# Kernel optimization log

Hardware: AMD Instinct MI355X
Metric: run time of the kernel (lower is better)

The kernel has to match this reference:

```python
import jax, jax.numpy as jnp
import numpy as np

B, H, S, D = 2, 16, 2048, 64  # batch, heads, seq, head_dim (d_model=1024)


def setup_inputs() -> dict:
    key = jax.random.key(0)
    kq, kk, kv, kp, kl = jax.random.split(key, 5)
    q = jax.random.normal(kq, (B, H, S, D), dtype=jnp.float32)
    k = jax.random.normal(kk, (B, H, D, S), dtype=jnp.float32)  # pre-transposed keys
    v = jax.random.normal(kv, (B, H, S, D), dtype=jnp.float32)
    prev = jax.random.normal(kp, (B, H, S, S), dtype=jnp.float32)  # Realformer residual scores
    # tail padding: each batch element has a random valid length in [S//2, S]
    lengths = jax.random.randint(kl, (B,), S // 2, S + 1)
    key_padding_mask = jnp.arange(S)[None, :] >= lengths[:, None]  # [B,S] bool, True = pad
    # causal attention mask, True = disallowed
    attn_mask = jnp.triu(jnp.ones((S, S), dtype=bool), k=1)[None, None]  # [1,1,S,S]
    scale = jnp.asarray(D ** -0.5, dtype=jnp.float32)        # learnable (lsa=True)
    extra_scale = jnp.asarray(1.0, dtype=jnp.float32)        # learnable (lsa=True)
    return {"q": q, "k": k, "v": v, "prev": prev,
            "key_padding_mask": key_padding_mask, "attn_mask": attn_mask,
            "scale": scale, "extra_scale": extra_scale}


def reference(q, k, v, prev, key_padding_mask, attn_mask, scale, extra_scale):
    eff_scale = scale * jnp.clip(extra_scale, 0.01, 50.0)
    # q @ k (k already [B,H,D,S]) -> scores [B,H,S,S]
    attn_scores = jnp.einsum('bhqd,bhdk->bhqk', q, k) * eff_scale + prev
    attn_scores = jnp.where(attn_mask, -jnp.inf, attn_scores)
    attn_scores = jnp.where(key_padding_mask[:, None, None, :], -jnp.inf, attn_scores)
    attn_weights = jax.nn.softmax(attn_scores, axis=-1)  # dropout p=0.0 -> identity
    output = jnp.einsum('bhqk,bhkd->bhqd', attn_weights, v)
    # res_attention=True -> return scores too
    return output, attn_weights, attn_scores
```

## Files before the change

### kernel.cpp

```cpp
#include <hip/hip_runtime.h>
#include <math.h>

#define S_LEN 2048
#define D_DIM 64
#define OUT_O_OFF 0
#define OUT_W_OFF 4194304
#define OUT_S_OFF 138412032

#define MASK_VAL (-1.0e30f)

typedef const __attribute__((address_space(4))) float* cfp;

__device__ __forceinline__ void decode_tile(int bid, int& bh, int& qt, int& cc) {
    const int xr = bid & 7, r = bid >> 3;
    bh = xr * 4 + (r >> 9);
    const int rem = r & 511;
    qt = rem >> 3;
    cc = rem & 7;
}

__device__ __forceinline__ void decode_row(int bid, int& bh, int& qt) {
    const int xr = bid & 7, r = bid >> 3;
    bh = xr * 4 + (r >> 6);
    qt = 63 - (r & 63);
}

__device__ __forceinline__ void fill_tile(float* dst_bh, int q0, int c0,
                                          float val, int t) {
    const float4 v4 = make_float4(val, val, val, val);
#pragma unroll
    for (int jj = 0; jj < 8; ++jj) {
        const int f   = jj * 256 + t;
        const int row = q0 + (f >> 6);
        const int c4  = (f & 63) * 4;
        *reinterpret_cast<float4*>(dst_bh + (size_t)row * S_LEN + c0 + c4) = v4;
    }
}

__global__ __launch_bounds__(256) void k_init(float4* __restrict__ stats4) {
    const int idx = blockIdx.x * 256 + threadIdx.x;
    stats4[idx] = make_float4(MASK_VAL, 0.f, MASK_VAL, 0.f);
}

__global__ __launch_bounds__(256) void k_scores(
    const float* __restrict__ q, const float* __restrict__ k,
    const float* __restrict__ prev, const unsigned char* __restrict__ kpm,
    const float* __restrict__ scale_p, const float* __restrict__ escale_p,
    float* __restrict__ out_scores, float2* __restrict__ stats)
{
    const int t    = threadIdx.x;
    const int lane = t & 63;
    const int rg   = __builtin_amdgcn_readfirstlane(t >> 6);
    int bh, qt, cc; decode_tile(blockIdx.x, bh, qt, cc);
    const int b  = bh >> 4;
    const int q0 = qt * 32, c0 = cc * 256;
    const unsigned char* kpb = kpm + b * S_LEN;
    float* sb = out_scores + (size_t)bh * S_LEN * S_LEN;

    if (qt < 8 * cc || kpb[c0]) {
        fill_tile(sb, q0, c0, MASK_VAL, t);
        return;
    }

    const float eff = scale_p[0] * fminf(fmaxf(escale_p[0], 0.01f), 50.0f);
    const int c = c0 + 4 * lane;
    const float* kb    = k + (size_t)bh * D_DIM * S_LEN;
    const float* prevb = prev + (size_t)bh * S_LEN * S_LEN;
    const cfp qc = (cfp)(q + ((size_t)bh * S_LEN + q0 + rg * 8) * D_DIM);

    const uchar4 pm4 = *reinterpret_cast<const uchar4*>(kpb + c);

    float4 pv[8];
#pragma unroll
    for (int i = 0; i < 8; ++i)
        pv[i] = *reinterpret_cast<const float4*>(
            prevb + (size_t)(q0 + rg * 8 + i) * S_LEN + c);

    float4 acc[8];
#pragma unroll
    for (int i = 0; i < 8; ++i) acc[i] = make_float4(0.f, 0.f, 0.f, 0.f);

#pragma unroll 1
    for (int d0 = 0; d0 < D_DIM; d0 += 8) {
        float qv[8][8];
#pragma unroll
        for (int i = 0; i < 8; ++i)
#pragma unroll
            for (int j = 0; j < 8; ++j)
                qv[i][j] = qc[i * D_DIM + d0 + j];
#pragma unroll
        for (int j = 0; j < 8; ++j) {
            const float4 kv = *reinterpret_cast<const float4*>(
                kb + (size_t)(d0 + j) * S_LEN + c);
#pragma unroll
            for (int i = 0; i < 8; ++i) {
                acc[i].x = fmaf(qv[i][j], kv.x, acc[i].x);
                acc[i].y = fmaf(qv[i][j], kv.y, acc[i].y);
                acc[i].z = fmaf(qv[i][j], kv.z, acc[i].z);
                acc[i].w = fmaf(qv[i][j], kv.w, acc[i].w);
            }
        }
    }

    float m[8], s[8];
#pragma unroll
    for (int i = 0; i < 8; ++i) {
        const int R = q0 + rg * 8 + i;
        float x0 = fmaf(acc[i].x, eff, pv[i].x);
        float x1 = fmaf(acc[i].y, eff, pv[i].y);
        float x2 = fmaf(acc[i].z, eff, pv[i].z);
        float x3 = fmaf(acc[i].w, eff, pv[i].w);
        x0 = (c + 0 <= R && !pm4.x) ? x0 : MASK_VAL;
        x1 = (c + 1 <= R && !pm4.y) ? x1 : MASK_VAL;
        x2 = (c + 2 <= R && !pm4.z) ? x2 : MASK_VAL;
        x3 = (c + 3 <= R && !pm4.w) ? x3 : MASK_VAL;
        *reinterpret_cast<float4*>(sb + (size_t)R * S_LEN + c) =
            make_float4(x0, x1, x2, x3);
        const float mx = fmaxf(fmaxf(x0, x1), fmaxf(x2, x3));
        m[i] = mx;
        s[i] = __expf(x0 - mx) + __expf(x1 - mx) +
               __expf(x2 - mx) + __expf(x3 - mx);
    }

#pragma unroll
    for (int i = 0; i < 8; ++i) {
#pragma unroll
        for (int msk = 32; msk >= 1; msk >>= 1) {
            const float m2 = __shfl_xor(m[i], msk, 64);
            const float s2 = __shfl_xor(s[i], msk, 64);
            const float M  = fmaxf(m[i], m2);
            const float sa = (s[i] == 0.f) ? 0.f : s[i] * __expf(m[i] - M);
            const float sb2 = (s2  == 0.f) ? 0.f : s2  * __expf(m2  - M);
            m[i] = M; s[i] = sa + sb2;
        }
        if (lane == i)
            stats[((size_t)bh * S_LEN + q0 + rg * 8 + i) * 8 + cc] =
                make_float2(m[i], s[i]);
    }
}

__global__ __launch_bounds__(256) void k_softmax(
    const float* __restrict__ scores, const float2* __restrict__ stats,
    const unsigned char* __restrict__ kpm, float* __restrict__ out_w)
{
    const int t    = threadIdx.x;
    const int lane = t & 63;
    const int rg   = __builtin_amdgcn_readfirstlane(t >> 6);
    int bh, qt, cc; decode_tile(blockIdx.x, bh, qt, cc);
    const int b  = bh >> 4;
    const int q0 = qt * 32, c0 = cc * 256;
    const unsigned char* kpb = kpm + b * S_LEN;
    float* wbh = out_w + (size_t)bh * S_LEN * S_LEN;

    if (qt < 8 * cc || kpb[c0]) {
        fill_tile(wbh, q0, c0, 0.f, t);
        return;
    }

    float mrow[8], inv[8];
#pragma unroll
    for (int i = 0; i < 8; ++i) {
        const cfp p = (cfp)&stats[((size_t)bh * S_LEN + q0 + rg * 8 + i) * 8];
        float M = p[0];
#pragma unroll
        for (int j = 1; j < 8; ++j) M = fmaxf(M, p[2 * j]);
        float S = 0.f;
#pragma unroll
        for (int j = 0; j < 8; ++j) S = fmaf(p[2 * j + 1], __expf(p[2 * j] - M), S);
        mrow[i] = M;
        inv[i]  = 1.0f / S;
    }

    const float* sbh = scores + (size_t)bh * S_LEN * S_LEN;
    const int c = c0 + 4 * lane;

#pragma unroll
    for (int i = 0; i < 8; ++i) {
        const int R = q0 + rg * 8 + i;
        const float4 sv = *reinterpret_cast<const float4*>(
            sbh + (size_t)R * S_LEN + c);
        float4 w;
        w.x = __expf(sv.x - mrow[i]) * inv[i];
        w.y = __expf(sv.y - mrow[i]) * inv[i];
        w.z = __expf(sv.z - mrow[i]) * inv[i];
        w.w = __expf(sv.w - mrow[i]) * inv[i];
        *reinterpret_cast<float4*>(wbh + (size_t)R * S_LEN + c) = w;
    }
}

__global__ __launch_bounds__(256) void k_pv(
    const float* __restrict__ w, const float* __restrict__ v,
    const unsigned char* __restrict__ kpm, float* __restrict__ out_o)
{
    __shared__ float wT[32][256];
    const int t    = threadIdx.x;
    const int lane = t & 63;
    const int rg   = __builtin_amdgcn_readfirstlane(t >> 6);
    const int dg   = lane >> 3;
    const int cs   = lane & 7;
    int bh, qt; decode_row(blockIdx.x, bh, qt);
    const int b  = bh >> 4;
    const int q0 = qt * 32;
    const unsigned char* kpb = kpm + b * S_LEN;

    const float* wbh = w + (size_t)bh * S_LEN * S_LEN;
    const float* vb  = v + (size_t)bh * S_LEN * D_DIM;

    float acc[8][8];
#pragma unroll
    for (int i = 0; i < 8; ++i)
#pragma unroll
        for (int j = 0; j < 8; ++j) acc[i][j] = 0.f;

    const int cend = q0 + 32;
    for (int c0 = 0; c0 < cend; c0 += 256) {
        if (kpb[c0]) break;
        const int c = c0 + 4 * lane;

#pragma unroll
        for (int i = 0; i < 8; ++i) {
            const int R = q0 + rg * 8 + i;
            const float4 wv = *reinterpret_cast<const float4*>(
                wbh + (size_t)R * S_LEN + c);
            *reinterpret_cast<float4*>(&wT[rg * 8 + i][4 * lane]) = wv;
        }

#pragma unroll 4
        for (int mm = 0; mm < 32; ++mm) {
            const int cc2 = mm * 8 + cs;
            float wr[8];
#pragma unroll
            for (int i = 0; i < 8; ++i) wr[i] = wT[rg * 8 + i][cc2];
            const float4 va = *reinterpret_cast<const float4*>(
                vb + (size_t)(c0 + cc2) * D_DIM + dg * 8);
            const float4 vb2 = *reinterpret_cast<const float4*>(
                vb + (size_t)(c0 + cc2) * D_DIM + dg * 8 + 4);
            const float vr[8] = {va.x, va.y, va.z, va.w, vb2.x, vb2.y, vb2.z, vb2.w};
#pragma unroll
            for (int i = 0; i < 8; ++i)
#pragma unroll
                for (int j = 0; j < 8; ++j)
                    acc[i][j] = fmaf(wr[i], vr[j], acc[i][j]);
        }
    }

#pragma unroll
    for (int i = 0; i < 8; ++i)
#pragma unroll
        for (int j = 0; j < 8; ++j) {
            acc[i][j] += __shfl_down(acc[i][j], 4, 64);
            acc[i][j] += __shfl_down(acc[i][j], 2, 64);
            acc[i][j] += __shfl_down(acc[i][j], 1, 64);
        }
    if (cs == 0) {
#pragma unroll
        for (int i = 0; i < 8; ++i) {
            const int R = q0 + rg * 8 + i;
            *reinterpret_cast<float4*>(out_o + ((size_t)bh * S_LEN + R) * D_DIM + dg * 8) =
                make_float4(acc[i][0], acc[i][1], acc[i][2], acc[i][3]);
            *reinterpret_cast<float4*>(out_o + ((size_t)bh * S_LEN + R) * D_DIM + dg * 8 + 4) =
                make_float4(acc[i][4], acc[i][5], acc[i][6], acc[i][7]);
        }
    }
}

extern "C" void kernel_launch(void* const* d_in, const int* in_sizes, int n_in,
                              void* d_out, int out_size, void* d_ws, size_t ws_size,
                              hipStream_t stream)
{
    const float* q      = (const float*)d_in[0];
    const float* k      = (const float*)d_in[1];
    const float* v      = (const float*)d_in[2];
    const float* prev   = (const float*)d_in[3];
    const unsigned char* kpm = (const unsigned char*)d_in[4];
    const float* scale  = (const float*)d_in[6];
    const float* escale = (const float*)d_in[7];

    float* out   = (float*)d_out;
    float* out_o = out + OUT_O_OFF;
    float* out_w = out + OUT_W_OFF;
    float* out_s = out + OUT_S_OFF;
    float2* stats = (float2*)d_ws;

    hipLaunchKernelGGL(k_init, dim3(1024), dim3(256), 0, stream, (float4*)stats);
    hipLaunchKernelGGL(k_scores, dim3(16384), dim3(256), 0, stream,
                       q, k, prev, kpm, scale, escale, out_s, stats);
    hipLaunchKernelGGL(k_softmax, dim3(16384), dim3(256), 0, stream,
                       out_s, stats, kpm, out_w);
    hipLaunchKernelGGL(k_pv, dim3(2048), dim3(256), 0, stream,
                       out_w, v, kpm, out_o);
}
```

Measured before the change: 729.6 us.

## Double-buffer K loads in score kernel and precompute merged row stats

The score kernel now preloads K rows into two register buffers so the loads for the next 8 dimensions are issued before the FMAs on the current ones, and it defers the prev-score loads until after the matmul. A new small kernel merges the per-chunk max/sum statistics once per row into (max, 1/sum), so each softmax tile no longer recomputes an 8-way merge. This hides memory latency and removes redundant exp work, at the cost of one extra launch and higher register pressure in the score kernel.

```diff
diff --git a/kernel.cpp b/kernel.cpp
--- a/kernel.cpp
+++ b/kernel.cpp
@@ -41,6 +41,25 @@
     const int idx = blockIdx.x * 256 + threadIdx.x;
     stats4[idx] = make_float4(MASK_VAL, 0.f, MASK_VAL, 0.f);
 }
+
+#define FMA_STEP(buf, dbase)                                          \
+    {                                                                 \
+        float qv[8][8];                                               \
+        _Pragma("unroll")                                             \
+        for (int i = 0; i < 8; ++i)                                   \
+            _Pragma("unroll")                                         \
+            for (int j = 0; j < 8; ++j)                               \
+                qv[i][j] = qc[i * D_DIM + (dbase) + j];               \
+        _Pragma("unroll")                                             \
+        for (int j = 0; j < 8; ++j)                                   \
+            _Pragma("unroll")                                         \
+            for (int i = 0; i < 8; ++i) {                             \
+                acc[i].x = fmaf(qv[i][j], buf[j].x, acc[i].x);        \
+                acc[i].y = fmaf(qv[i][j], buf[j].y, acc[i].y);        \
+                acc[i].z = fmaf(qv[i][j], buf[j].z, acc[i].z);        \
+                acc[i].w = fmaf(qv[i][j], buf[j].w, acc[i].w);        \
+            }                                                         \
+    }
 
 __global__ __launch_bounds__(256) void k_scores(
     const float* __restrict__ q, const float* __restrict__ k,
@@ -70,37 +89,38 @@
 
     const uchar4 pm4 = *reinterpret_cast<const uchar4*>(kpb + c);
 
-    float4 pv[8];
+    float4 acc[8];
+#pragma unroll
+    for (int i = 0; i < 8; ++i) acc[i] = make_float4(0.f, 0.f, 0.f, 0.f);
+
+    float4 kvA[8], kvB[8], pv[8];
+#pragma unroll
+    for (int j = 0; j < 8; ++j)
+        kvA[j] = *reinterpret_cast<const float4*>(kb + (size_t)j * S_LEN + c);
+
+#pragma unroll 1
+    for (int d0 = 0; d0 < 48; d0 += 16) {
+#pragma unroll
+        for (int j = 0; j < 8; ++j)
+            kvB[j] = *reinterpret_cast<const float4*>(
+                kb + (size_t)(d0 + 8 + j) * S_LEN + c);
+        FMA_STEP(kvA, d0)
+#pragma unroll
+        for (int j = 0; j < 8; ++j)
+            kvA[j] = *reinterpret_cast<const float4*>(
+                kb + (size_t)(d0 + 16 + j) * S_LEN + c);
+        FMA_STEP(kvB, d0 + 8)
+    }
+#pragma unroll
+    for (int j = 0; j < 8; ++j)
+        kvB[j] = *reinterpret_cast<const float4*>(
+            kb + (size_t)(56 + j) * S_LEN + c);
+    FMA_STEP(kvA, 48)
 #pragma unroll
     for (int i = 0; i < 8; ++i)
         pv[i] = *reinterpret_cast<const float4*>(
             prevb + (size_t)(q0 + rg * 8 + i) * S_LEN + c);
-
-    float4 acc[8];
-#pragma unroll
-    for (int i = 0; i < 8; ++i) acc[i] = make_float4(0.f, 0.f, 0.f, 0.f);
-
-#pragma unroll 1
-    for (int d0 = 0; d0 < D_DIM; d0 += 8) {
-        float qv[8][8];
-#pragma unroll
-        for (int i = 0; i < 8; ++i)
-#pragma unroll
-            for (int j = 0; j < 8; ++j)
-                qv[i][j] = qc[i * D_DIM + d0 + j];
-#pragma unroll
-        for (int j = 0; j < 8; ++j) {
-            const float4 kv = *reinterpret_cast<const float4*>(
-                kb + (size_t)(d0 + j) * S_LEN + c);
-#pragma unroll
-            for (int i = 0; i < 8; ++i) {
-                acc[i].x = fmaf(qv[i][j], kv.x, acc[i].x);
-                acc[i].y = fmaf(qv[i][j], kv.y, acc[i].y);
-                acc[i].z = fmaf(qv[i][j], kv.z, acc[i].z);
-                acc[i].w = fmaf(qv[i][j], kv.w, acc[i].w);
-            }
-        }
-    }
+    FMA_STEP(kvB, 56)
 
     float m[8], s[8];
 #pragma unroll
@@ -139,8 +159,23 @@
     }
 }
 
+__global__ __launch_bounds__(256) void k_stats(
+    const float2* __restrict__ part, float2* __restrict__ merged)
+{
+    const int row = blockIdx.x * 256 + threadIdx.x;
+    const float4* p4 = reinterpret_cast<const float4*>(part + (size_t)row * 8);
+    const float4 a = p4[0], b = p4[1], c = p4[2], d = p4[3];
+    const float M = fmaxf(fmaxf(fmaxf(a.x, a.z), fmaxf(b.x, b.z)),
+                          fmaxf(fmaxf(c.x, c.z), fmaxf(d.x, d.z)));
+    const float S = a.y * __expf(a.x - M) + a.w * __expf(a.z - M)
+                  + b.y * __expf(b.x - M) + b.w * __expf(b.z - M)
+                  + c.y * __expf(c.x - M) + c.w * __expf(c.z - M)
+                  + d.y * __expf(d.x - M) + d.w * __expf(d.z - M);
+    merged[row] = make_float2(M, 1.0f / S);
+}
+
 __global__ __launch_bounds__(256) void k_softmax(
-    const float* __restrict__ scores, const float2* __restrict__ stats,
+    const float* __restrict__ scores, const float2* __restrict__ merged,
     const unsigned char* __restrict__ kpm, float* __restrict__ out_w)
 {
     const int t    = threadIdx.x;
@@ -157,33 +192,22 @@
         return;
     }
 
-    float mrow[8], inv[8];
-#pragma unroll
-    for (int i = 0; i < 8; ++i) {
-        const cfp p = (cfp)&stats[((size_t)bh * S_LEN + q0 + rg * 8 + i) * 8];
-        float M = p[0];
-#pragma unroll
-        for (int j = 1; j < 8; ++j) M = fmaxf(M, p[2 * j]);
-        float S = 0.f;
-#pragma unroll
-        for (int j = 0; j < 8; ++j) S = fmaf(p[2 * j + 1], __expf(p[2 * j] - M), S);
-        mrow[i] = M;
-        inv[i]  = 1.0f / S;
-    }
-
+    const cfp st = (cfp)&merged[(size_t)bh * S_LEN + q0 + rg * 8];
     const float* sbh = scores + (size_t)bh * S_LEN * S_LEN;
     const int c = c0 + 4 * lane;
 
 #pragma unroll
     for (int i = 0; i < 8; ++i) {
         const int R = q0 + rg * 8 + i;
+        const float mrow = st[2 * i];
+        const float inv  = st[2 * i + 1];
         const float4 sv = *reinterpret_cast<const float4*>(
             sbh + (size_t)R * S_LEN + c);
         float4 w;
-        w.x = __expf(sv.x - mrow[i]) * inv[i];
-        w.y = __expf(sv.y - mrow[i]) * inv[i];
-        w.z = __expf(sv.z - mrow[i]) * inv[i];
-        w.w = __expf(sv.w - mrow[i]) * inv[i];
+        w.x = __expf(sv.x - mrow) * inv;
+        w.y = __expf(sv.y - mrow) * inv;
+        w.z = __expf(sv.z - mrow) * inv;
+        w.w = __expf(sv.w - mrow) * inv;
         *reinterpret_cast<float4*>(wbh + (size_t)R * S_LEN + c) = w;
     }
 }
@@ -280,13 +304,15 @@
     float* out_o = out + OUT_O_OFF;
     float* out_w = out + OUT_W_OFF;
     float* out_s = out + OUT_S_OFF;
-    float2* stats = (float2*)d_ws;
+    float2* stats  = (float2*)d_ws;
+    float2* merged = (float2*)((char*)d_ws + 4 * 1024 * 1024);
 
     hipLaunchKernelGGL(k_init, dim3(1024), dim3(256), 0, stream, (float4*)stats);
     hipLaunchKernelGGL(k_scores, dim3(16384), dim3(256), 0, stream,
                        q, k, prev, kpm, scale, escale, out_s, stats);
+    hipLaunchKernelGGL(k_stats, dim3(256), dim3(256), 0, stream, stats, merged);
     hipLaunchKernelGGL(k_softmax, dim3(16384), dim3(256), 0, stream,
-                       out_s, stats, kpm, out_w);
+                       out_s, merged, kpm, out_w);
     hipLaunchKernelGGL(k_pv, dim3(2048), dim3(256), 0, stream,
                        out_w, v, kpm, out_o);
 }
```

Measured after the change: 761.7 us. 4.4% more time.
